# Optimization experiments

Measured on AMD Instinct MI355X. Metric: run time of the kernel, lower is better.

## Reference

```python
import jax, jax.numpy as jnp
import numpy as np

B, L, E, H = 4, 2048, 512, 8


def setup_inputs() -> dict:
    key = jax.random.key(0)
    ks = jax.random.split(key, 12)
    s = 0.02
    inp = {
        "values": jax.random.normal(ks[0], (B, L, E), jnp.float32),
        "keys": jax.random.normal(ks[1], (B, L, E), jnp.float32),
        "queries": jax.random.normal(ks[2], (B, L, E), jnp.float32),
    }
    mask = jax.random.randint(ks[3], (B, L, H, H), 0, 2, jnp.int32)
    # guarantee at least one unmasked entry per softmax row to avoid NaN rows
    mask = mask.at[..., 0].set(1)
    inp["mask"] = mask
    # Linear(E, E*H) weights stored as (in, out); torch uses y = x @ W.T + b
    inp["Wv"] = jax.random.normal(ks[4], (E, E * H), jnp.float32) * s
    inp["bv"] = jnp.zeros((E * H,), jnp.float32)
    inp["Wk"] = jax.random.normal(ks[5], (E, E * H), jnp.float32) * s
    inp["bk"] = jnp.zeros((E * H,), jnp.float32)
    inp["Wq"] = jax.random.normal(ks[6], (E, E * H), jnp.float32) * s
    inp["bq"] = jnp.zeros((E * H,), jnp.float32)
    inp["Wo"] = jax.random.normal(ks[7], (E * H, E), jnp.float32) * s
    inp["bo"] = jnp.zeros((E,), jnp.float32)
    return inp


def reference(values, keys, queries, mask, Wv, bv, Wk, bk, Wq, bq, Wo, bo):
    b, l, e = queries.shape
    h = Wq.shape[1] // e

    def proj(x, W, bias):
        # (B,L,E) -> (B,L,H,E) -> transpose(1,2) -> (B,H,L,E)
        return (x @ W + bias).reshape(b, -1, h, e).transpose(0, 2, 1, 3)

    v = proj(values, Wv, bv)
    k = proj(keys, Wk, bk)
    q = proj(queries, Wq, bq)
    # Faithful to source: einsum labels applied to the TRANSPOSED (B,H,L,E)
    # tensors, so 'q'/'k' bind to the heads axis and 'h' binds to seq axis.
    # energy: (B, L, H, H) -- head-vs-head scores at each position.
    energy = jnp.einsum('nqhd,nkhd->nhqk', q, k)
    energy = jnp.where(mask == 0, -jnp.inf, energy)
    attn = jax.nn.softmax(energy / jnp.sqrt(jnp.float32(e)), axis=3)
    # out of einsum: (B, H, L, E); raw row-major reshape to (B, L, H*E)
    out = jnp.einsum('nhql,nlhd->nqhd', attn, v).reshape(b, -1, h * e)
    return out @ Wo + bo
```

## Files before the change

kernel.cpp:

```cpp
#include <hip/hip_runtime.h>
#include <stdint.h>

typedef __attribute__((ext_vector_type(4))) float f32x4;
typedef __attribute__((ext_vector_type(8))) __bf16 bf16x8;

__device__ __forceinline__ unsigned short f2bf(float f) {
  union { float f; uint32_t u; } v; v.f = f;
  uint32_t u = v.u;
  return (unsigned short)((u + 0x7FFFu + ((u >> 16) & 1u)) >> 16);
}
__device__ __forceinline__ float bflo(uint32_t u) {
  union { uint32_t u; float f; } v; v.u = u << 16; return v.f;
}
__device__ __forceinline__ float bfhi(uint32_t u) {
  union { uint32_t u; float f; } v; v.u = u & 0xffff0000u; return v.f;
}

__device__ __forceinline__ void async_copy16(void* lds, const void* g) {
  __builtin_amdgcn_global_load_lds(
      (const __attribute__((address_space(1))) void*)g,
      (__attribute__((address_space(3))) void*)lds,
      16, 0, 0);
}

__global__ void cvt3_f32_bf16(const float* __restrict__ in0,
                              const float* __restrict__ in1,
                              const float* __restrict__ in2,
                              uint32_t* __restrict__ out, int n) {
  const float* in = (blockIdx.y == 0) ? in0 : (blockIdx.y == 1) ? in1 : in2;
  uint32_t* o = out + (size_t)blockIdx.y * (n / 2);
  int i = blockIdx.x * blockDim.x + threadIdx.x;
  int idx = i * 8;
  if (idx >= n) return;
  float4 a = *(const float4*)(in + idx);
  float4 b = *(const float4*)(in + idx + 4);
  uint4 ov;
  ov.x = f2bf(a.x) | ((uint32_t)f2bf(a.y) << 16);
  ov.y = f2bf(a.z) | ((uint32_t)f2bf(a.w) << 16);
  ov.z = f2bf(b.x) | ((uint32_t)f2bf(b.y) << 16);
  ov.w = f2bf(b.z) | ((uint32_t)f2bf(b.w) << 16);
  *(uint4*)(o + i * 4) = ov;
}

__global__ void transpose3_to_bf16(const float* __restrict__ in0,
                                   const float* __restrict__ in1,
                                   const float* __restrict__ in2,
                                   unsigned short* __restrict__ out,
                                   int R, int C) {
  const float* in = (blockIdx.z == 0) ? in0 : (blockIdx.z == 1) ? in1 : in2;
  unsigned short* o = out + (size_t)blockIdx.z * ((size_t)R * C);
  __shared__ float tile[32][33];
  int c0 = blockIdx.x * 32, r0 = blockIdx.y * 32;
  int tx = threadIdx.x, ty = threadIdx.y;
  #pragma unroll
  for (int rr = 0; rr < 32; rr += 8)
    tile[ty + rr][tx] = in[(size_t)(r0 + ty + rr) * C + c0 + tx];
  __syncthreads();
  #pragma unroll
  for (int rr = 0; rr < 32; rr += 8)
    o[(size_t)(c0 + ty + rr) * R + r0 + tx] = f2bf(tile[tx][ty + rr]);
}

__global__ void transpose_to_bf16(const float* __restrict__ in,
                                  unsigned short* __restrict__ out,
                                  int R, int C) {
  __shared__ float tile[32][33];
  int c0 = blockIdx.x * 32, r0 = blockIdx.y * 32;
  int tx = threadIdx.x, ty = threadIdx.y;
  #pragma unroll
  for (int rr = 0; rr < 32; rr += 8)
    tile[ty + rr][tx] = in[(size_t)(r0 + ty + rr) * C + c0 + tx];
  __syncthreads();
  #pragma unroll
  for (int rr = 0; rr < 32; rr += 8)
    out[(size_t)(c0 + ty + rr) * R + r0 + tx] = f2bf(tile[tx][ty + rr]);
}

template <int NK, bool PARTIAL>
__global__ __launch_bounds__(512, 2) void gemm256(
    const unsigned short* __restrict__ A,
    const unsigned short* __restrict__ Bt,
    const float* __restrict__ bias,
    void* __restrict__ Cout,
    int Mt, int Nt, int KC, int Kfull) {
  static_assert(NK >= 3, "schedule needs >=3 K-tiles");
  __shared__ unsigned short lds[2 * 2 * 256 * 64];

  const int nwg = Mt * Nt * KC;
  const int cpx = nwg >> 3;
  const int bid = blockIdx.x;
  const int nb = (bid & 7) * cpx + (bid >> 3);
  const int bm = nb % Mt;
  const int rest = nb / Mt;
  const int bn = rest % Nt;
  const int kc = rest / Nt;
  const int N = Nt * 256;
  const size_t koff = (size_t)kc * (NK * 64);

  const int tid = threadIdx.x;
  const int wv = tid >> 6, ln = tid & 63;
  const int wm = wv >> 2, wn = wv & 3;

  f32x4 acc[8][4] = {};
  bf16x8 af[4][2];
  bf16x8 bfb[2][2];

  auto stage_A = [&](int h, int tt) {
    #pragma unroll
    for (int r = 0; r < 2; ++r) {
      const int rb = r * 128 + h * 64 + wv * 8;
      const int row = rb + (ln >> 3);
      const int kcs = (ln & 7) ^ (row & 7);
      const unsigned short* g =
          A + (size_t)(bm * 256 + row) * Kfull + koff + tt * 64 + kcs * 8;
      char* dst = (char*)lds + (size_t)(tt & 1) * 65536 + rb * 128;
      async_copy16(dst, g);
    }
  };
  auto stage_B = [&](int h, int tt) {
    #pragma unroll
    for (int r = 0; r < 2; ++r) {
      const int s = r * 2 + (wv >> 2);
      const int rb = s * 64 + h * 32 + (wv & 3) * 8;
      const int row = rb + (ln >> 3);
      const int kcs = (ln & 7) ^ (row & 7);
      const unsigned short* g =
          Bt + (size_t)(bn * 256 + row) * Kfull + koff + tt * 64 + kcs * 8;
      char* dst = (char*)lds + (size_t)(tt & 1) * 65536 + 32768 + rb * 128;
      async_copy16(dst, g);
    }
  };
  auto load_af = [&](int mh, const char* buf) {
    #pragma unroll
    for (int f = 0; f < 4; ++f) {
      const int lr = wm * 128 + (mh * 4 + f) * 16 + (ln & 15);
      #pragma unroll
      for (int s = 0; s < 2; ++s) {
        const int kq = s * 4 + (ln >> 4);
        af[f][s] = *(const bf16x8*)(buf + lr * 128 + ((kq ^ (lr & 7)) * 16));
      }
    }
  };
  auto load_bf = [&](int nh, const char* buf) {
    #pragma unroll
    for (int gq = 0; gq < 2; ++gq) {
      const int lr = wn * 64 + (nh * 2 + gq) * 16 + (ln & 15);
      #pragma unroll
      for (int s = 0; s < 2; ++s) {
        const int kq = s * 4 + (ln >> 4);
        bfb[gq][s] =
            *(const bf16x8*)(buf + 32768 + lr * 128 + ((kq ^ (lr & 7)) * 16));
      }
    }
  };
  auto mfma_quad = [&](int mh, int nh) {
    __builtin_amdgcn_sched_barrier(0);
    __builtin_amdgcn_s_barrier();
    __builtin_amdgcn_sched_barrier(0);
    __builtin_amdgcn_s_setprio(1);
    #pragma unroll
    for (int f = 0; f < 4; ++f)
      #pragma unroll
      for (int gq = 0; gq < 2; ++gq)
        #pragma unroll
        for (int s = 0; s < 2; ++s)
          acc[mh * 4 + f][nh * 2 + gq] = __builtin_amdgcn_mfma_f32_16x16x32_bf16(
              bfb[gq][s], af[f][s], acc[mh * 4 + f][nh * 2 + gq], 0, 0, 0);
    __builtin_amdgcn_s_setprio(0);
    __builtin_amdgcn_sched_barrier(0);
  };

  stage_A(0, 0); stage_B(1, 0); stage_A(1, 0); stage_B(0, 0);
  stage_A(0, 1); stage_B(1, 1); stage_A(1, 1);
  asm volatile("s_waitcnt vmcnt(6)" ::: "memory");
  __builtin_amdgcn_sched_barrier(0);
  __builtin_amdgcn_s_barrier();

  for (int t = 0; t < NK; ++t) {
    const char* buf = (const char*)lds + (size_t)(t & 1) * 65536;
    load_af(0, buf); load_bf(0, buf);
    if (t + 1 < NK) stage_B(0, t + 1);
    mfma_quad(0, 0);
    __builtin_amdgcn_s_barrier();
    load_bf(1, buf);
    if (t + 2 < NK) stage_A(0, t + 2);
    mfma_quad(0, 1);
    __builtin_amdgcn_s_barrier();
    load_af(1, buf);
    if (t + 2 < NK) stage_B(1, t + 2);
    mfma_quad(1, 1);
    __builtin_amdgcn_s_barrier();
    load_bf(0, buf);
    if (t + 2 < NK) stage_A(1, t + 2);
    mfma_quad(1, 0);
    if (t + 2 < NK) {
      asm volatile("s_waitcnt vmcnt(6)" ::: "memory");
    } else if (t + 1 < NK) {
      asm volatile("s_waitcnt vmcnt(0)" ::: "memory");
    }
    __builtin_amdgcn_sched_barrier(0);
    __builtin_amdgcn_s_barrier();
  }

  const int m0 = bm * 256 + wm * 128 + (ln & 15);
  const int n0 = bn * 256 + wn * 64 + ((ln >> 4) << 2);
  if (PARTIAL) {
    float* Cp = (float*)Cout + (size_t)kc * ((size_t)Mt * 256) * N;
    #pragma unroll
    for (int f = 0; f < 8; ++f) {
      const int row = m0 + f * 16;
      #pragma unroll
      for (int g = 0; g < 4; ++g)
        *(f32x4*)(Cp + (size_t)row * N + n0 + g * 16) = acc[f][g];
    }
  } else {
    unsigned short* C = (unsigned short*)Cout;
    #pragma unroll
    for (int f = 0; f < 8; ++f) {
      const int row = m0 + f * 16;
      #pragma unroll
      for (int g = 0; g < 4; ++g) {
        const int col = n0 + g * 16;
        float4 bv = *(const float4*)(bias + col);
        uint2 o;
        o.x = f2bf(acc[f][g][0] + bv.x) | ((uint32_t)f2bf(acc[f][g][1] + bv.y) << 16);
        o.y = f2bf(acc[f][g][2] + bv.z) | ((uint32_t)f2bf(acc[f][g][3] + bv.w) << 16);
        *(uint2*)(C + (size_t)row * N + col) = o;
      }
    }
  }
}

__global__ void reduce4_bias(const float* __restrict__ p,
                             const float* __restrict__ bo,
                             float* __restrict__ out) {
  const size_t S = (size_t)8192 * 512;
  size_t i = ((size_t)blockIdx.x * 256 + threadIdx.x) * 4;
  float4 a = *(const float4*)(p + i);
  float4 b = *(const float4*)(p + S + i);
  float4 c = *(const float4*)(p + 2 * S + i);
  float4 d = *(const float4*)(p + 3 * S + i);
  float4 bb = *(const float4*)(bo + (int)(i & 511));
  float4 o;
  o.x = a.x + b.x + c.x + d.x + bb.x;
  o.y = a.y + b.y + c.y + d.y + bb.y;
  o.z = a.z + b.z + c.z + d.z + bb.z;
  o.w = a.w + b.w + c.w + d.w + bb.w;
  *(float4*)(out + i) = o;
}

__global__ __launch_bounds__(256) void energy_mfma(
    const unsigned short* __restrict__ Q,
    const unsigned short* __restrict__ Kb,
    const int* __restrict__ mask,
    float* __restrict__ P) {
  const int wave = threadIdx.x >> 6, ln = threadIdx.x & 63;
  const int t2 = (blockIdx.x * 4 + wave) * 2;
  const int r16 = ln & 15;
  const int g = ln >> 4;
  const size_t rowoff = (size_t)(t2 + (r16 >> 3)) * 4096 + (r16 & 7) * 512 + g * 8;
  const unsigned short* qb = Q + rowoff;
  const unsigned short* kb = Kb + rowoff;

  f32x4 acc = {};
  #pragma unroll
  for (int s = 0; s < 16; ++s) {
    bf16x8 qf = *(const bf16x8*)(qb + s * 32);
    bf16x8 kf = *(const bf16x8*)(kb + s * 32);
    acc = __builtin_amdgcn_mfma_f32_16x16x32_bf16(qf, kf, acc, 0, 0, 0);
  }

  const int ct = r16 >> 3, j = r16 & 7;
  const bool valid = ((g >> 1) == ct);
  const int tok = t2 + ct;
  float pv[4];
  #pragma unroll
  for (int r = 0; r < 4; ++r) {
    const int i = (g & 1) * 4 + r;
    float e = acc[r] * 0.044194173824159216f;
    int mk = 1;
    if (valid) mk = mask[(size_t)tok * 64 + i * 8 + j];
    if (mk == 0) e = -1e30f;
    float m = e;
    m = fmaxf(m, __shfl_xor(m, 1, 64));
    m = fmaxf(m, __shfl_xor(m, 2, 64));
    m = fmaxf(m, __shfl_xor(m, 4, 64));
    float p = __expf(e - m);
    float sum = p;
    sum += __shfl_xor(sum, 1, 64);
    sum += __shfl_xor(sum, 2, 64);
    sum += __shfl_xor(sum, 4, 64);
    pv[r] = p / sum;
  }
  if (valid) {
    #pragma unroll
    for (int r = 0; r < 4; ++r) {
      const int i = (g & 1) * 4 + r;
      P[(size_t)tok * 64 + i * 8 + j] = pv[r];
    }
  }
}

__global__ __launch_bounds__(256) void pv_kernel(
    const float* __restrict__ P,
    const unsigned short* __restrict__ Vb,
    unsigned short* __restrict__ out2) {
  const int wave = threadIdx.x >> 6, lane = threadIdx.x & 63;
  const int t = blockIdx.x * 4 + wave;
  const unsigned short* Vr = Vb + (size_t)t * 4096;
  float att = P[(size_t)t * 64 + lane];

  uint4 v4[8];
  #pragma unroll
  for (int jj = 0; jj < 8; ++jj)
    v4[jj] = *(const uint4*)(Vr + jj * 512 + lane * 8);

  const int nb = t >> 11, l = t & 2047;
  const size_t tok_base = (size_t)nb * 8388608 + (size_t)(l >> 3) * 4096 +
                          (size_t)(l & 7) * 512 + lane * 8;
  #pragma unroll
  for (int hh = 0; hh < 8; ++hh) {
    float accv[8] = {0.f, 0.f, 0.f, 0.f, 0.f, 0.f, 0.f, 0.f};
    #pragma unroll
    for (int jj = 0; jj < 8; ++jj) {
      float a = __shfl(att, hh * 8 + jj, 64);
      accv[0] += a * bflo(v4[jj].x); accv[1] += a * bfhi(v4[jj].x);
      accv[2] += a * bflo(v4[jj].y); accv[3] += a * bfhi(v4[jj].y);
      accv[4] += a * bflo(v4[jj].z); accv[5] += a * bfhi(v4[jj].z);
      accv[6] += a * bflo(v4[jj].w); accv[7] += a * bfhi(v4[jj].w);
    }
    uint4 o;
    o.x = f2bf(accv[0]) | ((uint32_t)f2bf(accv[1]) << 16);
    o.y = f2bf(accv[2]) | ((uint32_t)f2bf(accv[3]) << 16);
    o.z = f2bf(accv[4]) | ((uint32_t)f2bf(accv[5]) << 16);
    o.w = f2bf(accv[6]) | ((uint32_t)f2bf(accv[7]) << 16);
    *(uint4*)(out2 + tok_base + (size_t)hh * 1048576) = o;
  }
}

extern "C" void kernel_launch(void* const* d_in, const int* in_sizes, int n_in,
                              void* d_out, int out_size, void* d_ws, size_t ws_size,
                              hipStream_t stream) {
  const float* values  = (const float*)d_in[0];
  const float* keys    = (const float*)d_in[1];
  const float* queries = (const float*)d_in[2];
  const int*   mask    = (const int*)d_in[3];
  const float* Wv = (const float*)d_in[4];
  const float* bv = (const float*)d_in[5];
  const float* Wk = (const float*)d_in[6];
  const float* bk = (const float*)d_in[7];
  const float* Wq = (const float*)d_in[8];
  const float* bq = (const float*)d_in[9];
  const float* Wo = (const float*)d_in[10];
  const float* bo = (const float*)d_in[11];

  unsigned short* xv  = (unsigned short*)d_ws;
  unsigned short* xk  = xv + 8192 * 512;
  unsigned short* xq  = xk + 8192 * 512;
  unsigned short* Wvt = xq + 8192 * 512;
  unsigned short* Wkt = Wvt + 4096 * 512;
  unsigned short* Wqt = Wkt + 4096 * 512;
  unsigned short* Wot = Wqt + 4096 * 512;
  float*          P   = (float*)(Wot + 4096 * 512);
  unsigned short* bufA = (unsigned short*)(P + 8192 * 64);
  unsigned short* bufB = bufA + (size_t)8192 * 4096;

  const int nx = 8192 * 512;
  cvt3_f32_bf16<<<dim3(nx / 8 / 256, 3), 256, 0, stream>>>(
      values, keys, queries, (uint32_t*)xv, nx);

  transpose3_to_bf16<<<dim3(4096 / 32, 512 / 32, 3), dim3(32, 8), 0, stream>>>(
      Wv, Wk, Wq, Wvt, 512, 4096);
  transpose_to_bf16<<<dim3(512 / 32, 4096 / 32), dim3(32, 8), 0, stream>>>(
      Wo, Wot, 4096, 512);

  gemm256<8, false><<<512, 512, 0, stream>>>(xq, Wqt, bq, bufA, 32, 16, 1, 512);
  gemm256<8, false><<<512, 512, 0, stream>>>(xk, Wkt, bk, bufB, 32, 16, 1, 512);

  energy_mfma<<<8192 / 8, 256, 0, stream>>>(bufA, bufB, mask, P);

  gemm256<8, false><<<512, 512, 0, stream>>>(xv, Wvt, bv, bufA, 32, 16, 1, 512);

  pv_kernel<<<8192 / 4, 256, 0, stream>>>(P, bufA, bufB);

  gemm256<16, true><<<256, 512, 0, stream>>>(bufB, Wot, nullptr, (float*)bufA,
                                             32, 2, 4, 4096);
  reduce4_bias<<<4096, 256, 0, stream>>>((float*)bufA, bo, (float*)d_out);
}
```

Baseline: 276.5 us.

## Make GEMM workgroups persistent over two N tiles with continuous pipeline

Each projection GEMM workgroup now computes two consecutive 256-wide N tiles. The K-loop pipeline runs straight across the tile boundary, so loads for the next tile are prefetched while the current tile finishes and writes its epilogue. This halves the grid from 512 to 256 workgroups, cutting pipeline prologue/drain overhead and fitting the grid to one wave of CUs. The cost is less parallelism, plus epilogue stores that now sit inside the main loop.

```diff
diff --git a/kernel.cpp b/kernel.cpp
--- a/kernel.cpp
+++ b/kernel.cpp
@@ -76,25 +76,26 @@
     out[(size_t)(c0 + ty + rr) * R + r0 + tx] = f2bf(tile[tx][ty + rr]);
 }
 
-template <int NK, bool PARTIAL>
+template <int NK, int NN, bool PARTIAL>
 __global__ __launch_bounds__(512, 2) void gemm256(
     const unsigned short* __restrict__ A,
     const unsigned short* __restrict__ Bt,
     const float* __restrict__ bias,
     void* __restrict__ Cout,
-    int Mt, int Nt, int KC, int Kfull) {
-  static_assert(NK >= 3, "schedule needs >=3 K-tiles");
+    int Mt, int NtG, int KC, int Kfull) {
+  constexpr int TT = NK * NN;
+  static_assert(TT >= 3, "schedule needs >=3 tiles");
   __shared__ unsigned short lds[2 * 2 * 256 * 64];
 
-  const int nwg = Mt * Nt * KC;
+  const int nwg = Mt * NtG * KC;
   const int cpx = nwg >> 3;
   const int bid = blockIdx.x;
   const int nb = (bid & 7) * cpx + (bid >> 3);
-  const int bm = nb % Mt;
-  const int rest = nb / Mt;
-  const int bn = rest % Nt;
-  const int kc = rest / Nt;
-  const int N = Nt * 256;
+  const int kc = nb / (Mt * NtG);
+  const int r2 = nb % (Mt * NtG);
+  const int bm = r2 / NtG;
+  const int ng = r2 % NtG;
+  const int N = NtG * NN * 256;
   const size_t koff = (size_t)kc * (NK * 64);
 
   const int tid = threadIdx.x;
@@ -105,19 +106,22 @@
   bf16x8 af[4][2];
   bf16x8 bfb[2][2];
 
-  auto stage_A = [&](int h, int tt) {
+  auto stage_A = [&](int h, int tau) {
+    const int kt = tau % NK;
     #pragma unroll
     for (int r = 0; r < 2; ++r) {
       const int rb = r * 128 + h * 64 + wv * 8;
       const int row = rb + (ln >> 3);
       const int kcs = (ln & 7) ^ (row & 7);
       const unsigned short* g =
-          A + (size_t)(bm * 256 + row) * Kfull + koff + tt * 64 + kcs * 8;
-      char* dst = (char*)lds + (size_t)(tt & 1) * 65536 + rb * 128;
+          A + (size_t)(bm * 256 + row) * Kfull + koff + kt * 64 + kcs * 8;
+      char* dst = (char*)lds + (size_t)(tau & 1) * 65536 + rb * 128;
       async_copy16(dst, g);
     }
   };
-  auto stage_B = [&](int h, int tt) {
+  auto stage_B = [&](int h, int tau) {
+    const int kt = tau % NK;
+    const int bnn = ng * NN + tau / NK;
     #pragma unroll
     for (int r = 0; r < 2; ++r) {
       const int s = r * 2 + (wv >> 2);
@@ -125,8 +129,8 @@
       const int row = rb + (ln >> 3);
       const int kcs = (ln & 7) ^ (row & 7);
       const unsigned short* g =
-          Bt + (size_t)(bn * 256 + row) * Kfull + koff + tt * 64 + kcs * 8;
-      char* dst = (char*)lds + (size_t)(tt & 1) * 65536 + 32768 + rb * 128;
+          Bt + (size_t)(bnn * 256 + row) * Kfull + koff + kt * 64 + kcs * 8;
+      char* dst = (char*)lds + (size_t)(tau & 1) * 65536 + 32768 + rb * 128;
       async_copy16(dst, g);
     }
   };
@@ -169,6 +173,40 @@
     __builtin_amdgcn_s_setprio(0);
     __builtin_amdgcn_sched_barrier(0);
   };
+  auto epilogue = [&](int nt) {
+    const int m0 = bm * 256 + wm * 128 + (ln & 15);
+    const int n0 = (ng * NN + nt) * 256 + wn * 64 + ((ln >> 4) << 2);
+    if (PARTIAL) {
+      float* Cp = (float*)Cout + (size_t)kc * ((size_t)Mt * 256) * N;
+      #pragma unroll
+      for (int f = 0; f < 8; ++f) {
+        const int row = m0 + f * 16;
+        #pragma unroll
+        for (int g = 0; g < 4; ++g)
+          *(f32x4*)(Cp + (size_t)row * N + n0 + g * 16) = acc[f][g];
+      }
+    } else {
+      unsigned short* C = (unsigned short*)Cout;
+      #pragma unroll
+      for (int f = 0; f < 8; ++f) {
+        const int row = m0 + f * 16;
+        #pragma unroll
+        for (int g = 0; g < 4; ++g) {
+          const int col = n0 + g * 16;
+          float4 bv = *(const float4*)(bias + col);
+          uint2 o;
+          o.x = f2bf(acc[f][g][0] + bv.x) | ((uint32_t)f2bf(acc[f][g][1] + bv.y) << 16);
+          o.y = f2bf(acc[f][g][2] + bv.z) | ((uint32_t)f2bf(acc[f][g][3] + bv.w) << 16);
+          *(uint2*)(C + (size_t)row * N + col) = o;
+        }
+      }
+    }
+    #pragma unroll
+    for (int f = 0; f < 8; ++f)
+      #pragma unroll
+      for (int g = 0; g < 4; ++g)
+        acc[f][g] = (f32x4){0.f, 0.f, 0.f, 0.f};
+  };
 
   stage_A(0, 0); stage_B(1, 0); stage_A(1, 0); stage_B(0, 0);
   stage_A(0, 1); stage_B(1, 1); stage_A(1, 1);
@@ -176,58 +214,31 @@
   __builtin_amdgcn_sched_barrier(0);
   __builtin_amdgcn_s_barrier();
 
-  for (int t = 0; t < NK; ++t) {
-    const char* buf = (const char*)lds + (size_t)(t & 1) * 65536;
+  for (int tau = 0; tau < TT; ++tau) {
+    const char* buf = (const char*)lds + (size_t)(tau & 1) * 65536;
     load_af(0, buf); load_bf(0, buf);
-    if (t + 1 < NK) stage_B(0, t + 1);
+    if (tau + 1 < TT) stage_B(0, tau + 1);
     mfma_quad(0, 0);
     __builtin_amdgcn_s_barrier();
     load_bf(1, buf);
-    if (t + 2 < NK) stage_A(0, t + 2);
+    if (tau + 2 < TT) stage_A(0, tau + 2);
     mfma_quad(0, 1);
     __builtin_amdgcn_s_barrier();
     load_af(1, buf);
-    if (t + 2 < NK) stage_B(1, t + 2);
+    if (tau + 2 < TT) stage_B(1, tau + 2);
     mfma_quad(1, 1);
     __builtin_amdgcn_s_barrier();
     load_bf(0, buf);
-    if (t + 2 < NK) stage_A(1, t + 2);
+    if (tau + 2 < TT) stage_A(1, tau + 2);
     mfma_quad(1, 0);
-    if (t + 2 < NK) {
+    if (tau + 2 < TT) {
       asm volatile("s_waitcnt vmcnt(6)" ::: "memory");
-    } else if (t + 1 < NK) {
+    } else if (tau + 1 < TT) {
       asm volatile("s_waitcnt vmcnt(0)" ::: "memory");
     }
     __builtin_amdgcn_sched_barrier(0);
     __builtin_amdgcn_s_barrier();
-  }
-
-  const int m0 = bm * 256 + wm * 128 + (ln & 15);
-  const int n0 = bn * 256 + wn * 64 + ((ln >> 4) << 2);
-  if (PARTIAL) {
-    float* Cp = (float*)Cout + (size_t)kc * ((size_t)Mt * 256) * N;
-    #pragma unroll
-    for (int f = 0; f < 8; ++f) {
-      const int row = m0 + f * 16;
-      #pragma unroll
-      for (int g = 0; g < 4; ++g)
-        *(f32x4*)(Cp + (size_t)row * N + n0 + g * 16) = acc[f][g];
-    }
-  } else {
-    unsigned short* C = (unsigned short*)Cout;
-    #pragma unroll
-    for (int f = 0; f < 8; ++f) {
-      const int row = m0 + f * 16;
-      #pragma unroll
-      for (int g = 0; g < 4; ++g) {
-        const int col = n0 + g * 16;
-        float4 bv = *(const float4*)(bias + col);
-        uint2 o;
-        o.x = f2bf(acc[f][g][0] + bv.x) | ((uint32_t)f2bf(acc[f][g][1] + bv.y) << 16);
-        o.y = f2bf(acc[f][g][2] + bv.z) | ((uint32_t)f2bf(acc[f][g][3] + bv.w) << 16);
-        *(uint2*)(C + (size_t)row * N + col) = o;
-      }
-    }
+    if ((tau + 1) % NK == 0) epilogue(tau / NK);
   }
 }
 
@@ -374,16 +385,16 @@
   transpose_to_bf16<<<dim3(512 / 32, 4096 / 32), dim3(32, 8), 0, stream>>>(
       Wo, Wot, 4096, 512);
 
-  gemm256<8, false><<<512, 512, 0, stream>>>(xq, Wqt, bq, bufA, 32, 16, 1, 512);
-  gemm256<8, false><<<512, 512, 0, stream>>>(xk, Wkt, bk, bufB, 32, 16, 1, 512);
+  gemm256<8, 2, false><<<256, 512, 0, stream>>>(xq, Wqt, bq, bufA, 32, 8, 1, 512);
+  gemm256<8, 2, false><<<256, 512, 0, stream>>>(xk, Wkt, bk, bufB, 32, 8, 1, 512);
 
   energy_mfma<<<8192 / 8, 256, 0, stream>>>(bufA, bufB, mask, P);
 
-  gemm256<8, false><<<512, 512, 0, stream>>>(xv, Wvt, bv, bufA, 32, 16, 1, 512);
+  gemm256<8, 2, false><<<256, 512, 0, stream>>>(xv, Wvt, bv, bufA, 32, 8, 1, 512);
 
   pv_kernel<<<8192 / 4, 256, 0, stream>>>(P, bufA, bufB);
 
-  gemm256<16, true><<<256, 512, 0, stream>>>(bufB, Wot, nullptr, (float*)bufA,
-                                             32, 2, 4, 4096);
+  gemm256<16, 1, true><<<256, 512, 0, stream>>>(bufB, Wot, nullptr, (float*)bufA,
+                                                32, 2, 4, 4096);
   reduce4_bias<<<4096, 256, 0, stream>>>((float*)bufA, bo, (float*)d_out);
 }
```

After: 271.6 us. Within noise of the previous version (-1.8%).
